# Kernel optimization log

Measured on AMD Instinct MI355X. Metric: run time of the kernel, lower is better.

## Reference

```python
import jax, jax.numpy as jnp
import numpy as np

N_ATOMS = 4096
BOX = 37.0
CUTOFF = 5.0


def _f_r(r, fe, beta, re, lam):
    # f_e * exp(-beta*(r/r_e - 1)) / (1 + (r/r_e - lamda)^20)
    x = r / re
    return fe * jnp.exp(-beta * (x - 1.0)) / (1.0 + (x - lam) ** 20)


def _phi_r(r, a, b, re, alpha, beta, kappa, lam):
    x = r / re
    l = a * jnp.exp(-alpha * (x - 1.0)) / (1.0 + (x - kappa) ** 20)
    rr = b * jnp.exp(-beta * (x - 1.0)) / (1.0 + (x - lam) ** 20)
    return l - rr


def setup_inputs() -> dict:
    key = jax.random.key(0)
    k1, k2 = jax.random.split(key)
    # coordinates in a box sized for metal-like density so neighbors exist within cutoff
    coords = jax.random.uniform(k1, (N_ATOMS, 3), dtype=jnp.float32) * BOX
    # all 22 EAM parameters positive in [1.0, 2.5] (r_e, rho_s, rho_n, rho_0, eta must be > 0)
    params = 1.0 + 1.5 * jax.random.uniform(k2, (N_ATOMS, 22), dtype=jnp.float32)
    return {"coords": coords, "params": params}


def reference(coords, params):
    N = coords.shape[0]
    # docstring column order: r_e, f_e, rho_e, rho_s, alpha, beta, A, B, kappa, lamda,
    # f_n0..f_n3, f_0..f_3, eta, f_e2, rho_n, rho_0
    r_e, f_e, rho_e, rho_s = params[:, 0], params[:, 1], params[:, 2], params[:, 3]
    alpha, beta = params[:, 4], params[:, 5]
    A, B, kappa, lam = params[:, 6], params[:, 7], params[:, 8], params[:, 9]
    eta, f_e2 = params[:, 18], params[:, 19]
    rho_n, rho_0 = params[:, 20], params[:, 21]

    # ---- full pairwise distances (safe diagonal for differentiable sqrt) ----
    diff = coords[None, :, :] - coords[:, None, :]            # [N, N, 3]
    r2 = jnp.sum(diff * diff, axis=-1)                        # [N, N]
    eye = jnp.eye(N, dtype=bool)
    r_mat = jnp.sqrt(jnp.where(eye, 1.0, r2))                 # [N, N]

    # ---- pair energy over i<j with r <= cutoff (masked, same math as torch filtering) ----
    iu, ju = jnp.triu_indices(N, k=1)                         # P = N(N-1)/2 pairs
    r_pair = r_mat[iu, ju]
    mask = r_pair <= CUTOFF
    r_safe = jnp.where(mask, r_pair, 1.0)                     # nan-safe for masked-out pairs

    fr_i = _f_r(r_safe, f_e[iu], beta[iu], r_e[iu], lam[iu])
    fr_j = _f_r(r_safe, f_e[ju], beta[ju], r_e[ju], lam[ju])
    ph_i = _phi_r(r_safe, A[iu], B[iu], r_e[iu], alpha[iu], beta[iu], kappa[iu], lam[iu])
    ph_j = _phi_r(r_safe, A[ju], B[ju], r_e[ju], alpha[ju], beta[ju], kappa[ju], lam[ju])
    phi_01 = fr_j / fr_i * ph_i + fr_i / fr_j * ph_j
    p_e = 0.5 * jnp.sum(jnp.where(mask, phi_01, 0.0))

    # ---- per-atom density rho_i = sum_{j != i} f_r(r_ij, params_j) (no cutoff, as in source) ----
    fr_mat = _f_r(r_mat, f_e[None, :], beta[None, :], r_e[None, :], lam[None, :])
    rho = jnp.sum(jnp.where(eye, 0.0, fr_mat), axis=1)        # [N]

    # ---- embedding F(rho) with three branches (if/elif/else -> nested where) ----
    xn = rho / rho_n - 1.0
    poly_n = params[:, 10] + params[:, 11] * xn + params[:, 12] * xn ** 2 + params[:, 13] * xn ** 3
    xe = rho / rho_e - 1.0
    poly_0 = params[:, 14] + params[:, 15] * xe + params[:, 16] * xe ** 2 + params[:, 17] * xe ** 3
    t = (rho / rho_s) ** eta
    tail = f_e2 * (1.0 - jnp.log(t)) * t
    F_i = jnp.where(rho < rho_n, poly_n, jnp.where(rho < rho_0, poly_0, tail))

    return p_e + jnp.sum(F_i)
```

## Files before the change

kernel.cpp:

```cpp
#include <hip/hip_runtime.h>
#include <math.h>

#define N_ATOMS 4096
#define NTILE   16
#define NJ      128
#define JT      32
#define LOG2E   1.4426950408889634f
#define LN2     0.6931471805599453f

typedef float v2f __attribute__((ext_vector_type(2)));

__device__ __forceinline__ float pow20f(float t) {
    float t2 = t * t, t4 = t2 * t2, t8 = t4 * t4, t16 = t8 * t8;
    return t16 * t4;
}

__device__ __forceinline__ float block_reduce(float v, float* red) {
    __syncthreads();
    #pragma unroll
    for (int off = 32; off > 0; off >>= 1) v += __shfl_down(v, off, 64);
    if ((threadIdx.x & 63) == 0) red[threadIdx.x >> 6] = v;
    __syncthreads();
    return (red[0] + red[1]) + (red[2] + red[3]);
}

__global__ __launch_bounds__(256) void pack_kernel(
    const float* __restrict__ coords, const float* __restrict__ params,
    float* __restrict__ apk, float* __restrict__ rpk)
{
    const int a = blockIdx.x * 256 + threadIdx.x;
    const float* p = params + 22 * a;
    const float x = coords[3*a], y = coords[3*a+1], z = coords[3*a+2];
    const float re = p[0], fe = p[1], be = p[5], al = p[4], la = p[9];
    const float rei  = __builtin_amdgcn_rcpf(re);
    const float bl2  = be * LOG2E;
    const float al2  = al * LOG2E;
    const float l2fe = __builtin_amdgcn_logf(fe);

    float lo = la + 1.0f, hi = la + 6.0f;
    #pragma unroll 1
    for (int it = 0; it < 28; ++it) {
        const float mid = 0.5f * (lo + hi);
        const float t   = mid - la;
        const float g   = l2fe - bl2 * (mid - 1.0f)
                        - __builtin_amdgcn_logf(1.0f + pow20f(t)) + 19.93f;
        if (g > 0.0f) lo = mid; else hi = mid;
    }
    const float rc  = re * hi;
    const float rc2 = fmaxf(rc * rc, 25.01f);

    float4* ad = (float4*)(apk + 12 * a);
    ad[0] = { x, y, z, rei };
    ad[1] = { -bl2 * rei, bl2 + l2fe, -la, p[7] * __builtin_amdgcn_rcpf(fe) };
    ad[2] = { -al2 * rei, al2, -p[8], p[6] };

    float* rd = rpk + 8 * (a >> 1) + (a & 1);
    rd[0] = x; rd[2] = y; rd[4] = z; rd[6] = rc2;
}

__global__ __launch_bounds__(256) void eam_main(
    const float* __restrict__ apk, const float* __restrict__ rpk,
    float* __restrict__ rho_part,
    float* __restrict__ e_part)
{
    __shared__ float4 srho4[JT / 2 * 2];
    __shared__ float4 sphi4[JT * 3];
    __shared__ float red[4];

    const int tid = threadIdx.x;
    const int bi  = blockIdx.x;
    const int s   = blockIdx.y;
    const int i   = bi * 256 + tid;
    const int jbase = s * JT;

    if (tid < 32)                     srho4[tid]      = ((const float4*)rpk)[s * 32 + tid];
    else if (tid >= 64 && tid < 160)  sphi4[tid - 64] = ((const float4*)apk)[s * 96 + (tid - 64)];

    const float4* apk4 = (const float4*)apk;
    const float4 a0 = apk4[i * 3 + 0];
    const float4 a1 = apk4[i * 3 + 1];
    const float4 a2 = apk4[i * 3 + 2];

    __syncthreads();

    const v2f xi2 = { a0.x, a0.x }, yi2 = { a0.y, a0.y }, zi2 = { a0.z, a0.z };
    unsigned int hits = 0u;

    #pragma unroll 4
    for (int k = 0; k < JT / 2; ++k) {
        const float4 f0 = srho4[k * 2 + 0];
        const float4 f1 = srho4[k * 2 + 1];
        const v2f x01 = { f0.x, f0.y }, y01 = { f0.z, f0.w };
        const v2f z01 = { f1.x, f1.y };
        const v2f dx = x01 - xi2, dy = y01 - yi2, dz = z01 - zi2;
        const v2f r2v = dx * dx + dy * dy + dz * dz;
        if (r2v.x <= f1.z) hits |= (1u << (2 * k));
        if (r2v.y <= f1.w) hits |= (1u << (2 * k + 1));
    }

    const int t = i - jbase;
    float rho = 0.0f;
    unsigned int phim = 0u;

    {
        unsigned int m = hits;
        if (t >= 0 && t < JT) m &= ~(1u << t);
        while (m) {
            const int k = __builtin_ctz(m);
            m &= m - 1;
            const float4 q0 = sphi4[k * 3 + 0];
            const float4 q1 = sphi4[k * 3 + 1];
            const float dx = q0.x - a0.x, dy = q0.y - a0.y, dz = q0.z - a0.z;
            const float r2 = fmaf(dx, dx, fmaf(dy, dy, dz * dz));
            const float r  = __builtin_amdgcn_sqrtf(r2);
            const float fr = __builtin_amdgcn_exp2f(fmaf(r, q1.x, q1.y))
                           * __builtin_amdgcn_rcpf(1.0f + pow20f(fmaf(r, q0.w, q1.z)));
            rho += fr;
            if (r2 <= 25.0f && k > t) phim |= (1u << k);
        }
    }
    rho_part[(size_t)s * N_ATOMS + i] = rho;

    float e = 0.0f;
    while (phim) {
        const int k = __builtin_ctz(phim);
        phim &= phim - 1;
        const float4 q0 = sphi4[k * 3 + 0];
        const float4 q1 = sphi4[k * 3 + 1];
        const float4 q2 = sphi4[k * 3 + 2];
        const float dx = q0.x - a0.x, dy = q0.y - a0.y, dz = q0.z - a0.z;
        const float r = __builtin_amdgcn_sqrtf(fmaf(dx, dx, fmaf(dy, dy, dz * dz)));

        const float fri = __builtin_amdgcn_exp2f(fmaf(r, a1.x, a1.y))
                        * __builtin_amdgcn_rcpf(1.0f + pow20f(fmaf(r, a0.w, a1.z)));
        const float frj = __builtin_amdgcn_exp2f(fmaf(r, q1.x, q1.y))
                        * __builtin_amdgcn_rcpf(1.0f + pow20f(fmaf(r, q0.w, q1.z)));
        const float ph_i = a2.w * __builtin_amdgcn_exp2f(fmaf(r, a2.x, a2.y))
                                * __builtin_amdgcn_rcpf(1.0f + pow20f(fmaf(r, a0.w, a2.z)))
                         - a1.w * fri;
        const float ph_j = q2.w * __builtin_amdgcn_exp2f(fmaf(r, q2.x, q2.y))
                                * __builtin_amdgcn_rcpf(1.0f + pow20f(fmaf(r, q0.w, q2.z)))
                         - q1.w * frj;
        e += 0.5f * fmaf(frj * frj, ph_i, fri * fri * ph_j)
                  * __builtin_amdgcn_rcpf(fri * frj);
    }

    const float eb = block_reduce(e, red);
    if (tid == 0) e_part[bi * NJ + s] = eb;
}

__global__ __launch_bounds__(1024) void eam_embed(
    const float* __restrict__ params,
    const float* __restrict__ rho_part, const float* __restrict__ e_part,
    float* __restrict__ tile_sum)
{
    __shared__ float acc[4][256];
    __shared__ float red16[16];
    const int tid = threadIdx.x;
    const int b   = blockIdx.x;
    const int al  = tid & 255;
    const int q   = tid >> 8;
    const int i   = b * 256 + al;

    float part = 0.0f;
    #pragma unroll 8
    for (int s = q * 32; s < q * 32 + 32; ++s)
        part += rho_part[(size_t)s * N_ATOMS + i];
    acc[q][al] = part;
    __syncthreads();

    float v = 0.0f;
    if (tid < 256) {
        const float rhoi = (acc[0][tid] + acc[1][tid]) + (acc[2][tid] + acc[3][tid]);
        const float* p = params + 22 * i;
        float F;
        if (rhoi < p[20]) {
            const float xn = rhoi / p[20] - 1.0f;
            F = p[10] + xn * (p[11] + xn * (p[12] + xn * p[13]));
        } else if (rhoi < p[21]) {
            const float xe = rhoi / p[2] - 1.0f;
            F = p[14] + xe * (p[15] + xe * (p[16] + xe * p[17]));
        } else {
            const float l2 = __builtin_amdgcn_logf(rhoi / p[3]);
            const float tt = __builtin_amdgcn_exp2f(p[18] * l2);
            const float lt = p[18] * l2 * LN2;
            F = p[19] * (1.0f - lt) * tt;
        }
        v = F + ((tid < NJ) ? e_part[b * NJ + tid] : 0.0f);
    }

    #pragma unroll
    for (int off = 32; off > 0; off >>= 1) v += __shfl_down(v, off, 64);
    if ((tid & 63) == 0) red16[tid >> 6] = v;
    __syncthreads();
    if (tid == 0) {
        float s = 0.0f;
        #pragma unroll
        for (int w = 0; w < 16; ++w) s += red16[w];
        tile_sum[b] = s;
    }
}

__global__ __launch_bounds__(64) void eam_final(
    const float* __restrict__ tile_sum, float* __restrict__ out)
{
    const int tid = threadIdx.x;
    float acc = (tid < NTILE) ? tile_sum[tid] : 0.0f;
    #pragma unroll
    for (int off = 8; off > 0; off >>= 1) acc += __shfl_down(acc, off, 64);
    if (tid == 0) out[0] = acc;
}

extern "C" void kernel_launch(void* const* d_in, const int* in_sizes, int n_in,
                              void* d_out, int out_size, void* d_ws, size_t ws_size,
                              hipStream_t stream) {
    const float* coords = (const float*)d_in[0];
    const float* params = (const float*)d_in[1];
    float* out = (float*)d_out;

    float* apk      = (float*)d_ws;
    float* rpk      = apk + (size_t)N_ATOMS * 12;
    float* rho_part = rpk + (size_t)(N_ATOMS / 2) * 8;
    float* e_part   = rho_part + (size_t)NJ * N_ATOMS;
    float* tile_sum = e_part + NTILE * NJ;

    pack_kernel<<<N_ATOMS / 256, 256, 0, stream>>>(coords, params, apk, rpk);
    dim3 grid(NTILE, NJ);
    eam_main<<<grid, 256, 0, stream>>>(apk, rpk, rho_part, e_part);
    eam_embed<<<NTILE, 1024, 0, stream>>>(params, rho_part, e_part, tile_sum);
    eam_final<<<1, 64, 0, stream>>>(tile_sum, out);
}
```

Measured before the change: 23.36 us.

## Widen j-tiles to 64 and fold final reduction into embed via atomic counter

Doubles the j-tile width per block to 64 atoms (64-bit hit masks), halving the number of j-slices and therefore the rho_part partials written and later summed. It also removes the separate final-reduction launch: the last embed block, found with an agent-scope atomic counter that the pack kernel resets, sums the tile partials and writes the output. Fewer blocks in the main kernel means less parallelism, roughly 1024 blocks instead of 2048, and longer serial bitmask loops per thread. The last-block pattern relies on correct acquire/release ordering of the tile_sum writes.

```diff
diff --git a/kernel.cpp b/kernel.cpp
--- a/kernel.cpp
+++ b/kernel.cpp
@@ -3,12 +3,13 @@
 
 #define N_ATOMS 4096
 #define NTILE   16
-#define NJ      128
-#define JT      32
+#define NJ      64
+#define JT      64
 #define LOG2E   1.4426950408889634f
 #define LN2     0.6931471805599453f
 
 typedef float v2f __attribute__((ext_vector_type(2)));
+typedef unsigned long long u64;
 
 __device__ __forceinline__ float pow20f(float t) {
     float t2 = t * t, t4 = t2 * t2, t8 = t4 * t4, t16 = t8 * t8;
@@ -26,8 +27,9 @@
 
 __global__ __launch_bounds__(256) void pack_kernel(
     const float* __restrict__ coords, const float* __restrict__ params,
-    float* __restrict__ apk, float* __restrict__ rpk)
+    float* __restrict__ apk, float* __restrict__ rpk, int* __restrict__ ctr)
 {
+    if (blockIdx.x == 0 && threadIdx.x == 0) *ctr = 0;
     const int a = blockIdx.x * 256 + threadIdx.x;
     const float* p = params + 22 * a;
     const float x = coords[3*a], y = coords[3*a+1], z = coords[3*a+2];
@@ -63,7 +65,7 @@
     float* __restrict__ rho_part,
     float* __restrict__ e_part)
 {
-    __shared__ float4 srho4[JT / 2 * 2];
+    __shared__ float4 srho4[JT];
     __shared__ float4 sphi4[JT * 3];
     __shared__ float red[4];
 
@@ -73,8 +75,8 @@
     const int i   = bi * 256 + tid;
     const int jbase = s * JT;
 
-    if (tid < 32)                     srho4[tid]      = ((const float4*)rpk)[s * 32 + tid];
-    else if (tid >= 64 && tid < 160)  sphi4[tid - 64] = ((const float4*)apk)[s * 96 + (tid - 64)];
+    if (tid < JT)       srho4[tid]      = ((const float4*)rpk)[s * JT + tid];
+    else                sphi4[tid - 64] = ((const float4*)apk)[s * 192 + (tid - 64)];
 
     const float4* apk4 = (const float4*)apk;
     const float4 a0 = apk4[i * 3 + 0];
@@ -84,7 +86,7 @@
     __syncthreads();
 
     const v2f xi2 = { a0.x, a0.x }, yi2 = { a0.y, a0.y }, zi2 = { a0.z, a0.z };
-    unsigned int hits = 0u;
+    u64 hits = 0ull;
 
     #pragma unroll 4
     for (int k = 0; k < JT / 2; ++k) {
@@ -94,19 +96,19 @@
         const v2f z01 = { f1.x, f1.y };
         const v2f dx = x01 - xi2, dy = y01 - yi2, dz = z01 - zi2;
         const v2f r2v = dx * dx + dy * dy + dz * dz;
-        if (r2v.x <= f1.z) hits |= (1u << (2 * k));
-        if (r2v.y <= f1.w) hits |= (1u << (2 * k + 1));
+        if (r2v.x <= f1.z) hits |= (1ull << (2 * k));
+        if (r2v.y <= f1.w) hits |= (1ull << (2 * k + 1));
     }
 
     const int t = i - jbase;
     float rho = 0.0f;
-    unsigned int phim = 0u;
+    u64 phim = 0ull;
 
     {
-        unsigned int m = hits;
-        if (t >= 0 && t < JT) m &= ~(1u << t);
+        u64 m = hits;
+        if (t >= 0 && t < JT) m &= ~(1ull << t);
         while (m) {
-            const int k = __builtin_ctz(m);
+            const int k = __builtin_ctzll(m);
             m &= m - 1;
             const float4 q0 = sphi4[k * 3 + 0];
             const float4 q1 = sphi4[k * 3 + 1];
@@ -116,14 +118,14 @@
             const float fr = __builtin_amdgcn_exp2f(fmaf(r, q1.x, q1.y))
                            * __builtin_amdgcn_rcpf(1.0f + pow20f(fmaf(r, q0.w, q1.z)));
             rho += fr;
-            if (r2 <= 25.0f && k > t) phim |= (1u << k);
+            if (r2 <= 25.0f && k > t) phim |= (1ull << k);
         }
     }
     rho_part[(size_t)s * N_ATOMS + i] = rho;
 
     float e = 0.0f;
     while (phim) {
-        const int k = __builtin_ctz(phim);
+        const int k = __builtin_ctzll(phim);
         phim &= phim - 1;
         const float4 q0 = sphi4[k * 3 + 0];
         const float4 q1 = sphi4[k * 3 + 1];
@@ -152,10 +154,12 @@
 __global__ __launch_bounds__(1024) void eam_embed(
     const float* __restrict__ params,
     const float* __restrict__ rho_part, const float* __restrict__ e_part,
-    float* __restrict__ tile_sum)
+    float* __restrict__ tile_sum,
+    int* __restrict__ ctr, float* __restrict__ out)
 {
     __shared__ float acc[4][256];
     __shared__ float red16[16];
+    __shared__ int sLast;
     const int tid = threadIdx.x;
     const int b   = blockIdx.x;
     const int al  = tid & 255;
@@ -163,8 +167,8 @@
     const int i   = b * 256 + al;
 
     float part = 0.0f;
-    #pragma unroll 8
-    for (int s = q * 32; s < q * 32 + 32; ++s)
+    #pragma unroll 4
+    for (int s = q * 16; s < q * 16 + 16; ++s)
         part += rho_part[(size_t)s * N_ATOMS + i];
     acc[q][al] = part;
     __syncthreads();
@@ -194,21 +198,22 @@
     if ((tid & 63) == 0) red16[tid >> 6] = v;
     __syncthreads();
     if (tid == 0) {
-        float s = 0.0f;
+        float sum = 0.0f;
         #pragma unroll
-        for (int w = 0; w < 16; ++w) s += red16[w];
-        tile_sum[b] = s;
-    }
-}
-
-__global__ __launch_bounds__(64) void eam_final(
-    const float* __restrict__ tile_sum, float* __restrict__ out)
-{
-    const int tid = threadIdx.x;
-    float acc = (tid < NTILE) ? tile_sum[tid] : 0.0f;
-    #pragma unroll
-    for (int off = 8; off > 0; off >>= 1) acc += __shfl_down(acc, off, 64);
-    if (tid == 0) out[0] = acc;
+        for (int w = 0; w < 16; ++w) sum += red16[w];
+        tile_sum[b] = sum;
+        int prev = __hip_atomic_fetch_add(ctr, 1, __ATOMIC_ACQ_REL,
+                                          __HIP_MEMORY_SCOPE_AGENT);
+        sLast = (prev == NTILE - 1);
+    }
+    __syncthreads();
+
+    if (sLast && tid == 0) {
+        float total = 0.0f;
+        #pragma unroll
+        for (int w = 0; w < NTILE; ++w) total += tile_sum[w];
+        out[0] = total;
+    }
 }
 
 extern "C" void kernel_launch(void* const* d_in, const int* in_sizes, int n_in,
@@ -223,10 +228,10 @@
     float* rho_part = rpk + (size_t)(N_ATOMS / 2) * 8;
     float* e_part   = rho_part + (size_t)NJ * N_ATOMS;
     float* tile_sum = e_part + NTILE * NJ;
-
-    pack_kernel<<<N_ATOMS / 256, 256, 0, stream>>>(coords, params, apk, rpk);
+    int*   ctr      = (int*)(tile_sum + NTILE);
+
+    pack_kernel<<<N_ATOMS / 256, 256, 0, stream>>>(coords, params, apk, rpk, ctr);
     dim3 grid(NTILE, NJ);
     eam_main<<<grid, 256, 0, stream>>>(apk, rpk, rho_part, e_part);
-    eam_embed<<<NTILE, 1024, 0, stream>>>(params, rho_part, e_part, tile_sum);
-    eam_final<<<1, 64, 0, stream>>>(tile_sum, out);
-}
+    eam_embed<<<NTILE, 1024, 0, stream>>>(params, rho_part, e_part, tile_sum, ctr, out);
+}
```

Measured after the change: 23.23 us. No clear change (-0.6%).
